# Performance work log

Measured on AMD Instinct MI355X. Metric: run time of the kernel, lower is better.

The kernel has to match this reference:

```python
import jax, jax.numpy as jnp
import numpy as np

D_MODEL = 1024
N_HEADS = 16
D_K = D_MODEL // N_HEADS


def setup_inputs() -> dict:
    key = jax.random.key(0)
    ks = jax.random.split(key, 12)
    B, S = 2, 2048
    scale = 1.0 / np.sqrt(D_MODEL)
    inp = {
        "query": jax.random.normal(ks[0], (B, S, D_MODEL), jnp.float32),
        "key": jax.random.normal(ks[1], (B, S, D_MODEL), jnp.float32),
        "value": jax.random.normal(ks[2], (B, S, D_MODEL), jnp.float32),
        "weights": jax.random.uniform(ks[3], (B, S), jnp.float32),
        "wq": jax.random.normal(ks[4], (D_MODEL, D_MODEL), jnp.float32) * scale,
        "bq": jnp.zeros((D_MODEL,), jnp.float32),
        "wk": jax.random.normal(ks[5], (D_MODEL, D_MODEL), jnp.float32) * scale,
        "bk": jnp.zeros((D_MODEL,), jnp.float32),
        "wv": jax.random.normal(ks[6], (D_MODEL, D_MODEL), jnp.float32) * scale,
        "bv": jnp.zeros((D_MODEL,), jnp.float32),
        "wo": jax.random.normal(ks[7], (D_MODEL, D_MODEL), jnp.float32) * scale,
        "bo": jnp.zeros((D_MODEL,), jnp.float32),
    }
    return inp


def _split_heads(x):
    # (B, S, d_model) -> (B, H, S, d_k)
    B, S, _ = x.shape
    return x.reshape(B, S, N_HEADS, D_K).transpose(0, 2, 1, 3)


def reference(query, key, value, weights, wq, bq, wk, bk, wv, bv, wo, bo):
    Q = _split_heads(query @ wq + bq)
    K = _split_heads(key @ wk + bk)
    V = _split_heads(value @ wv + bv)
    # scores: (B, H, n_q, n_kv)
    scores = jnp.einsum("bhqd,bhkd->bhqk", Q, K) / np.sqrt(D_K)
    log_w = jnp.log(weights + 1e-20)[:, None, None, :]  # (B,1,1,n_kv)
    attn = jax.nn.softmax(scores + log_w, axis=-1)
    out = jnp.einsum("bhqk,bhkd->bhqd", attn, V)
    B, H, S, Dk = out.shape
    out = out.transpose(0, 2, 1, 3).reshape(B, S, D_MODEL)
    return out @ wo + bo
```

## Files before the change

kernel.cpp:

```cpp
#include <hip/hip_runtime.h>

typedef unsigned short u16;
typedef __bf16 bf16x8 __attribute__((ext_vector_type(8)));
typedef float f32x4 __attribute__((ext_vector_type(4)));
typedef float f32x16 __attribute__((ext_vector_type(16)));

#define D_MODEL 1024
#define NH 16
#define DKD 64
#define BB 2
#define SS 2048
#define QSCL 0.18033688011112042f

#if __has_builtin(__builtin_amdgcn_exp2f)
#define EXP2(x) __builtin_amdgcn_exp2f(x)
#else
#define EXP2(x) exp2f(x)
#endif

__device__ __forceinline__ u16 f2bf(float f) {
  union { float f; unsigned u; } x; x.f = f;
  unsigned r = x.u + 0x7fffu + ((x.u >> 16) & 1u);
  return (u16)(r >> 16);
}

__device__ __forceinline__ void gld16(const u16* g, u16* l) {
  __builtin_amdgcn_global_load_lds((__attribute__((address_space(1))) void*)(g),
                                   (__attribute__((address_space(3))) void*)(l),
                                   16, 0, 0);
}

extern "C" __global__ void __launch_bounds__(256) kprep_conv(
    const float* __restrict__ q, const float* __restrict__ k, const float* __restrict__ v,
    u16* __restrict__ xq, u16* __restrict__ xk, u16* __restrict__ xv)
{
  int z = blockIdx.y;
  const float* s = z == 0 ? q : (z == 1 ? k : v);
  u16* d = z == 0 ? xq : (z == 1 ? xk : xv);
  int i = (blockIdx.x * 256 + threadIdx.x) * 4;
  float4 val = *(const float4*)(s + i);
  ushort4 o;
  o.x = f2bf(val.x); o.y = f2bf(val.y); o.z = f2bf(val.z); o.w = f2bf(val.w);
  *(ushort4*)(d + i) = o;
}

extern "C" __global__ void __launch_bounds__(256) kprep_wt(
    const float* __restrict__ w0, const float* __restrict__ w1,
    const float* __restrict__ w2, const float* __restrict__ w3,
    u16* __restrict__ o0, u16* __restrict__ o1, u16* __restrict__ o2, u16* __restrict__ o3)
{
  const float* src; u16* dst;
  switch (blockIdx.z) {
    case 0: src = w0; dst = o0; break;
    case 1: src = w1; dst = o1; break;
    case 2: src = w2; dst = o2; break;
    default: src = w3; dst = o3; break;
  }
  __shared__ float t[32][33];
  int n0 = blockIdx.x * 32, k0 = blockIdx.y * 32;
  int tx = threadIdx.x & 31, ty = threadIdx.x >> 5;
  #pragma unroll
  for (int i = 0; i < 32; i += 8)
    t[ty + i][tx] = src[(k0 + ty + i) * D_MODEL + n0 + tx];
  __syncthreads();
  #pragma unroll
  for (int i = 0; i < 32; i += 8)
    dst[(size_t)(n0 + ty + i) * D_MODEL + k0 + tx] = f2bf(t[tx][ty + i]);
}

extern "C" __global__ void __launch_bounds__(256) klw(
    const float* __restrict__ w, float* __restrict__ lw)
{
  int i = blockIdx.x * 256 + threadIdx.x;
  if (i < BB * SS) lw[i] = log2f(w[i] + 1e-20f) - 16.0f;
}

extern "C" __global__ void __launch_bounds__(256) ktrans_v(
    const u16* __restrict__ src, u16* __restrict__ dst)
{
  __shared__ u16 T[64][72];
  int bh = blockIdx.y; int s0 = blockIdx.x * 64;
  int tid = threadIdx.x;
  int r = tid >> 3, c = (tid & 7) * 8;
  #pragma unroll
  for (int i = 0; i < 2; ++i)
    *(bf16x8*)&T[r + i * 32][c] = *(const bf16x8*)&src[((size_t)bh * SS + s0 + r + i * 32) * DKD + c];
  __syncthreads();
  #pragma unroll
  for (int i = 0; i < 2; ++i) {
    int dk = r + i * 32;
    ushort4 o0, o1;
    o0.x = T[c + 0][dk]; o0.y = T[c + 1][dk]; o0.z = T[c + 2][dk]; o0.w = T[c + 3][dk];
    o1.x = T[c + 4][dk]; o1.y = T[c + 5][dk]; o1.z = T[c + 6][dk]; o1.w = T[c + 7][dk];
    *(ushort4*)&dst[((size_t)bh * DKD + dk) * SS + s0 + c] = o0;
    *(ushort4*)&dst[((size_t)bh * DKD + dk) * SS + s0 + c + 4] = o1;
  }
}

__device__ __forceinline__ void gemm_tile(const u16* __restrict__ Ag, const u16* __restrict__ Bg,
                                          u16* As, u16* Bs, f32x4 acc[4][4], int tid)
{
  int lane = tid & 63;
  int lr = lane & 15, lg = lane >> 4;
  int w = tid >> 6, wr = w >> 1, wc = w & 1;
  for (int k0 = 0; k0 < D_MODEL; k0 += 32) {
    #pragma unroll
    for (int c = 0; c < 2; ++c) {
      int idx = tid + c * 256;
      int row = idx >> 2, col = (idx & 3) * 8;
      gld16(Ag + row * D_MODEL + k0 + col, As + idx * 8);
      gld16(Bg + row * D_MODEL + k0 + col, Bs + idx * 8);
    }
    __syncthreads();
    bf16x8 af[4], bfr[4];
    #pragma unroll
    for (int mi = 0; mi < 4; ++mi)
      af[mi] = *(const bf16x8*)(As + (wr * 64 + mi * 16 + lr) * 32 + lg * 8);
    #pragma unroll
    for (int nj = 0; nj < 4; ++nj)
      bfr[nj] = *(const bf16x8*)(Bs + (wc * 64 + nj * 16 + lr) * 32 + lg * 8);
    #pragma unroll
    for (int mi = 0; mi < 4; ++mi)
      #pragma unroll
      for (int nj = 0; nj < 4; ++nj)
        acc[mi][nj] = __builtin_amdgcn_mfma_f32_16x16x32_bf16(af[mi], bfr[nj], acc[mi][nj], 0, 0, 0);
    __syncthreads();
  }
}

extern "C" __global__ void __launch_bounds__(256) kgemm_qkv(
    const u16* __restrict__ xq, const u16* __restrict__ xk, const u16* __restrict__ xv,
    const u16* __restrict__ wqt, const u16* __restrict__ wkt, const u16* __restrict__ wvt,
    const float* __restrict__ bq, const float* __restrict__ bk, const float* __restrict__ bv,
    u16* __restrict__ Qb, u16* __restrict__ Kb, u16* __restrict__ Vb)
{
  __shared__ u16 As[128 * 32], Bs[128 * 32];
  int z = blockIdx.z;
  const u16* X  = z == 0 ? xq : (z == 1 ? xk : xv);
  const u16* Wt = z == 0 ? wqt : (z == 1 ? wkt : wvt);
  const float* bias = z == 0 ? bq : (z == 1 ? bk : bv);
  u16* dst = z == 0 ? Qb : (z == 1 ? Kb : Vb);
  int tid = threadIdx.x;
  f32x4 zero = {0.f, 0.f, 0.f, 0.f};
  f32x4 acc[4][4];
  #pragma unroll
  for (int i = 0; i < 4; ++i)
    #pragma unroll
    for (int j = 0; j < 4; ++j) acc[i][j] = zero;
  int m0 = blockIdx.y * 128, n0 = blockIdx.x * 128;
  gemm_tile(X + (size_t)m0 * D_MODEL, Wt + (size_t)n0 * D_MODEL, As, Bs, acc, tid);
  int lane = tid & 63, lr = lane & 15, lg = lane >> 4;
  int w = tid >> 6, wr = w >> 1, wc = w & 1;
  float scl = (z == 0) ? QSCL : 1.0f;
  #pragma unroll
  for (int mi = 0; mi < 4; ++mi)
    #pragma unroll
    for (int nj = 0; nj < 4; ++nj) {
      int n = n0 + wc * 64 + nj * 16 + lr;
      float bs = bias[n];
      int h = n >> 6, dk = n & 63;
      #pragma unroll
      for (int j = 0; j < 4; ++j) {
        int m = m0 + wr * 64 + mi * 16 + lg * 4 + j;
        int b = m >> 11, s = m & 2047;
        dst[(((size_t)(b * NH + h)) * SS + s) * DKD + dk] = f2bf((acc[mi][nj][j] + bs) * scl);
      }
    }
}

extern "C" __global__ void __launch_bounds__(256) kgemm_o(
    const u16* __restrict__ AO, const u16* __restrict__ wot,
    const float* __restrict__ bo, float* __restrict__ out)
{
  __shared__ u16 As[128 * 32], Bs[128 * 32];
  int tid = threadIdx.x;
  f32x4 zero = {0.f, 0.f, 0.f, 0.f};
  f32x4 acc[4][4];
  #pragma unroll
  for (int i = 0; i < 4; ++i)
    #pragma unroll
    for (int j = 0; j < 4; ++j) acc[i][j] = zero;
  int m0 = blockIdx.y * 128, n0 = blockIdx.x * 128;
  gemm_tile(AO + (size_t)m0 * D_MODEL, wot + (size_t)n0 * D_MODEL, As, Bs, acc, tid);
  int lane = tid & 63, lr = lane & 15, lg = lane >> 4;
  int w = tid >> 6, wr = w >> 1, wc = w & 1;
  #pragma unroll
  for (int mi = 0; mi < 4; ++mi)
    #pragma unroll
    for (int nj = 0; nj < 4; ++nj) {
      int n = n0 + wc * 64 + nj * 16 + lr;
      float bs = bo[n];
      #pragma unroll
      for (int j = 0; j < 4; ++j) {
        int m = m0 + wr * 64 + mi * 16 + lg * 4 + j;
        out[(size_t)m * D_MODEL + n] = acc[mi][nj][j] + bs;
      }
    }
}

extern "C" __global__ void __launch_bounds__(256, 4) kattn(
    const u16* __restrict__ Qb, const u16* __restrict__ Kb, const u16* __restrict__ Vt,
    const float* __restrict__ lw2, u16* __restrict__ AO)
{
  __shared__ __align__(16) u16 Ks[2][64 * 64];
  __shared__ __align__(16) u16 Vs[2][64 * 64];
  __shared__ __align__(16) float lwf[SS];

  int tid = threadIdx.x, lane = tid & 63, w = tid >> 6;
  int lq = lane & 31, hi = lane >> 5;

  int n = blockIdx.x;
  int xcd = n & 7, slot = n >> 3;
  int bh = xcd + 8 * (slot >> 4);
  int q0 = (slot & 15) * 128;
  int b = bh >> 4, h = bh & 15;

  const u16* Qg = Qb + ((size_t)bh * SS + q0 + w * 32) * DKD;
  const u16* Kg = Kb + (size_t)bh * SS * DKD;
  const u16* Vg = Vt + (size_t)bh * DKD * SS;
  const float* lwb = lw2 + b * SS;

  #pragma unroll
  for (int i = 0; i < 2; ++i) {
    int idx = tid + i * 256;
    *(float4*)&lwf[idx * 4] = *(const float4*)(lwb + idx * 4);
  }

  bf16x8 qf[4];
  #pragma unroll
  for (int kc = 0; kc < 4; ++kc)
    qf[kc] = *(const bf16x8*)(Qg + lq * DKD + kc * 16 + hi * 8);

  f32x16 acco[2] = {};
  float lsp[4] = {0.f, 0.f, 0.f, 0.f};

  int srow0 = tid >> 3, sc0 = ((tid & 7) ^ (srow0 & 7)) * 8;
  int srow1 = srow0 + 32, sc1 = ((tid & 7) ^ (srow1 & 7)) * 8;

#define STAGE(t, bi) do { \
    gld16(Kg + (size_t)((t) * 64 + srow0) * DKD + sc0, &Ks[bi][tid * 8]); \
    gld16(Kg + (size_t)((t) * 64 + srow1) * DKD + sc1, &Ks[bi][(tid + 256) * 8]); \
    gld16(Vg + (size_t)srow0 * SS + (t) * 64 + sc0, &Vs[bi][tid * 8]); \
    gld16(Vg + (size_t)srow1 * SS + (t) * 64 + sc1, &Vs[bi][(tid + 256) * 8]); \
  } while (0)

  const int NT = SS / 64;
  STAGE(0, 0);
  for (int t = 0; t < NT; ++t) {
    asm volatile("s_waitcnt vmcnt(0) lgkmcnt(0)" ::: "memory");
    __builtin_amdgcn_s_barrier();
    __builtin_amdgcn_sched_barrier(0);
    if (t + 1 < NT) STAGE(t + 1, (t + 1) & 1);
    int bi = t & 1;
    int kv0 = t * 64;

    f32x16 st[2];
    #pragma unroll
    for (int nh = 0; nh < 2; ++nh)
      #pragma unroll
      for (int g = 0; g < 4; ++g) {
        f32x4 lv = *(const f32x4*)&lwf[kv0 + nh * 32 + 4 * hi + 8 * g];
        st[nh][4 * g + 0] = lv[0]; st[nh][4 * g + 1] = lv[1];
        st[nh][4 * g + 2] = lv[2]; st[nh][4 * g + 3] = lv[3];
      }

    __builtin_amdgcn_s_setprio(1);
    #pragma unroll
    for (int kc = 0; kc < 4; ++kc) {
      bf16x8 kf0 = *(const bf16x8*)&Ks[bi][(lq) * 64      + (((kc * 2 + hi) ^ (lq & 7)) * 8)];
      bf16x8 kf1 = *(const bf16x8*)&Ks[bi][(32 + lq) * 64 + (((kc * 2 + hi) ^ (lq & 7)) * 8)];
      st[0] = __builtin_amdgcn_mfma_f32_32x32x16_bf16(kf0, qf[kc], st[0], 0, 0, 0);
      st[1] = __builtin_amdgcn_mfma_f32_32x32x16_bf16(kf1, qf[kc], st[1], 0, 0, 0);
    }
    __builtin_amdgcn_s_setprio(0);

    unsigned wd[2][8];
    #pragma unroll
    for (int nh = 0; nh < 2; ++nh)
      #pragma unroll
      for (int r2 = 0; r2 < 8; ++r2) {
        float plo = EXP2(st[nh][2 * r2]);
        float phi = EXP2(st[nh][2 * r2 + 1]);
        lsp[r2 & 3] += plo + phi;
        union { unsigned u; __bf16 b2[2]; } cv;
        cv.b2[0] = (__bf16)plo; cv.b2[1] = (__bf16)phi;
        wd[nh][r2] = cv.u;
      }

    bf16x8 Pb[4];
    #pragma unroll
    for (int c = 0; c < 4; ++c) {
      int nh = c >> 1, j0 = 4 * (c & 1);
      auto s1 = __builtin_amdgcn_permlane32_swap(wd[nh][j0 + 0], wd[nh][j0 + 2], false, false);
      auto s2 = __builtin_amdgcn_permlane32_swap(wd[nh][j0 + 1], wd[nh][j0 + 3], false, false);
      union { unsigned u[4]; bf16x8 v; } pb;
      pb.u[0] = s1[0]; pb.u[1] = s2[0]; pb.u[2] = s1[1]; pb.u[3] = s2[1];
      Pb[c] = pb.v;
    }

    __builtin_amdgcn_s_setprio(1);
    #pragma unroll
    for (int c = 0; c < 4; ++c) {
      bf16x8 vf0 = *(const bf16x8*)&Vs[bi][(lq) * 64      + (((c * 2 + hi) ^ (lq & 7)) * 8)];
      bf16x8 vf1 = *(const bf16x8*)&Vs[bi][(32 + lq) * 64 + (((c * 2 + hi) ^ (lq & 7)) * 8)];
      acco[0] = __builtin_amdgcn_mfma_f32_32x32x16_bf16(vf0, Pb[c], acco[0], 0, 0, 0);
      acco[1] = __builtin_amdgcn_mfma_f32_32x32x16_bf16(vf1, Pb[c], acco[1], 0, 0, 0);
    }
    __builtin_amdgcn_s_setprio(0);
  }
#undef STAGE

  float lsum = (lsp[0] + lsp[1]) + (lsp[2] + lsp[3]);
  lsum += __shfl_xor(lsum, 32);
  float inv = 1.0f / lsum;
  int s = q0 + w * 32 + lq;
  size_t base = ((size_t)b * SS + s) * D_MODEL + h * DKD;
  #pragma unroll
  for (int dh = 0; dh < 2; ++dh)
    #pragma unroll
    for (int g = 0; g < 4; ++g) {
      ushort4 o;
      o.x = f2bf(acco[dh][4 * g + 0] * inv);
      o.y = f2bf(acco[dh][4 * g + 1] * inv);
      o.z = f2bf(acco[dh][4 * g + 2] * inv);
      o.w = f2bf(acco[dh][4 * g + 3] * inv);
      *(ushort4*)(AO + base + dh * 32 + 4 * hi + 8 * g) = o;
    }
}

extern "C" void kernel_launch(void* const* d_in, const int* in_sizes, int n_in,
                              void* d_out, int out_size, void* d_ws, size_t ws_size,
                              hipStream_t stream) {
  const float* query = (const float*)d_in[0];
  const float* key_  = (const float*)d_in[1];
  const float* value = (const float*)d_in[2];
  const float* wts   = (const float*)d_in[3];
  const float* wq = (const float*)d_in[4];
  const float* bq = (const float*)d_in[5];
  const float* wk = (const float*)d_in[6];
  const float* bk = (const float*)d_in[7];
  const float* wv = (const float*)d_in[8];
  const float* bv = (const float*)d_in[9];
  const float* wo = (const float*)d_in[10];
  const float* bo = (const float*)d_in[11];
  float* out = (float*)d_out;

  char* ws = (char*)d_ws;
  const size_t MB = 1024 * 1024;
  u16* Xq  = (u16*)(ws + 0 * MB);
  u16* Xk  = (u16*)(ws + 8 * MB);
  u16* Xv  = (u16*)(ws + 16 * MB);
  u16* WqT = (u16*)(ws + 24 * MB);
  u16* WkT = (u16*)(ws + 26 * MB);
  u16* WvT = (u16*)(ws + 28 * MB);
  u16* WoT = (u16*)(ws + 30 * MB);
  u16* Qb  = (u16*)(ws + 32 * MB);
  u16* Kb  = (u16*)(ws + 40 * MB);
  u16* Vb  = (u16*)(ws + 48 * MB);
  u16* AO  = (u16*)(ws + 56 * MB);
  float* lwbuf = (float*)(ws + 64 * MB);
  u16* VtT = (u16*)(ws + 16 * MB);

  kprep_conv<<<dim3(4096, 3), 256, 0, stream>>>(query, key_, value, Xq, Xk, Xv);
  kprep_wt<<<dim3(32, 32, 4), 256, 0, stream>>>(wq, wk, wv, wo, WqT, WkT, WvT, WoT);
  klw<<<16, 256, 0, stream>>>(wts, lwbuf);
  kgemm_qkv<<<dim3(8, 32, 3), 256, 0, stream>>>(Xq, Xk, Xv, WqT, WkT, WvT, bq, bk, bv, Qb, Kb, Vb);
  ktrans_v<<<dim3(32, 32), 256, 0, stream>>>(Vb, VtT);
  kattn<<<512, 256, 0, stream>>>(Qb, Kb, VtT, lwbuf, AO);
  kgemm_o<<<dim3(8, 32), 256, 0, stream>>>(AO, WoT, bo, out);
}
```

Before: 139.9 us.

## Split KV loop across two wave groups in attention and fuse log-weight prep

The attention kernel now runs 512 threads per block, with two groups of four waves each processing alternate KV tiles for the same queries. Partial accumulators and row sums are combined through shared memory at the end. K/V staging moves to a four-slot ring with a deeper prefetch. The separate log-weight kernel is folded into an extra block of the conversion kernel to save a launch. This should raise latency hiding and in-flight memory traffic, at the cost of more shared memory, an extra barrier per iteration and a final reduction.

```diff
diff --git a/kernel.cpp b/kernel.cpp
--- a/kernel.cpp
+++ b/kernel.cpp
@@ -32,9 +32,25 @@
 
 extern "C" __global__ void __launch_bounds__(256) kprep_conv(
     const float* __restrict__ q, const float* __restrict__ k, const float* __restrict__ v,
-    u16* __restrict__ xq, u16* __restrict__ xk, u16* __restrict__ xv)
+    const float* __restrict__ wts,
+    u16* __restrict__ xq, u16* __restrict__ xk, u16* __restrict__ xv,
+    float* __restrict__ lw)
 {
   int z = blockIdx.y;
+  if (blockIdx.x == 4096) {
+    if (z == 0) {
+      int i = threadIdx.x * 16;
+      #pragma unroll
+      for (int j = 0; j < 16; j += 4) {
+        float4 val = *(const float4*)(wts + i + j);
+        lw[i + j + 0] = log2f(val.x + 1e-20f) - 16.0f;
+        lw[i + j + 1] = log2f(val.y + 1e-20f) - 16.0f;
+        lw[i + j + 2] = log2f(val.z + 1e-20f) - 16.0f;
+        lw[i + j + 3] = log2f(val.w + 1e-20f) - 16.0f;
+      }
+    }
+    return;
+  }
   const float* s = z == 0 ? q : (z == 1 ? k : v);
   u16* d = z == 0 ? xq : (z == 1 ? xk : xv);
   int i = (blockIdx.x * 256 + threadIdx.x) * 4;
@@ -66,13 +82,6 @@
   #pragma unroll
   for (int i = 0; i < 32; i += 8)
     dst[(size_t)(n0 + ty + i) * D_MODEL + k0 + tx] = f2bf(t[tx][ty + i]);
-}
-
-extern "C" __global__ void __launch_bounds__(256) klw(
-    const float* __restrict__ w, float* __restrict__ lw)
-{
-  int i = blockIdx.x * 256 + threadIdx.x;
-  if (i < BB * SS) lw[i] = log2f(w[i] + 1e-20f) - 16.0f;
 }
 
 extern "C" __global__ void __launch_bounds__(256) ktrans_v(
@@ -198,16 +207,16 @@
     }
 }
 
-extern "C" __global__ void __launch_bounds__(256, 4) kattn(
+extern "C" __global__ void __launch_bounds__(512, 4) kattn(
     const u16* __restrict__ Qb, const u16* __restrict__ Kb, const u16* __restrict__ Vt,
     const float* __restrict__ lw2, u16* __restrict__ AO)
 {
-  __shared__ __align__(16) u16 Ks[2][64 * 64];
-  __shared__ __align__(16) u16 Vs[2][64 * 64];
-  __shared__ __align__(16) float lwf[SS];
+  __shared__ __align__(16) char smem[4 * 16384 + 8192];
+  float* lwf = (float*)(smem + 65536);
 
   int tid = threadIdx.x, lane = tid & 63, w = tid >> 6;
   int lq = lane & 31, hi = lane >> 5;
+  int qw = w & 3, par = w >> 2;
 
   int n = blockIdx.x;
   int xcd = n & 7, slot = n >> 3;
@@ -215,16 +224,12 @@
   int q0 = (slot & 15) * 128;
   int b = bh >> 4, h = bh & 15;
 
-  const u16* Qg = Qb + ((size_t)bh * SS + q0 + w * 32) * DKD;
+  const u16* Qg = Qb + ((size_t)bh * SS + q0 + qw * 32) * DKD;
   const u16* Kg = Kb + (size_t)bh * SS * DKD;
   const u16* Vg = Vt + (size_t)bh * DKD * SS;
   const float* lwb = lw2 + b * SS;
 
-  #pragma unroll
-  for (int i = 0; i < 2; ++i) {
-    int idx = tid + i * 256;
-    *(float4*)&lwf[idx * 4] = *(const float4*)(lwb + idx * 4);
-  }
+  *(float4*)&lwf[tid * 4] = *(const float4*)(lwb + tid * 4);
 
   bf16x8 qf[4];
   #pragma unroll
@@ -234,25 +239,27 @@
   f32x16 acco[2] = {};
   float lsp[4] = {0.f, 0.f, 0.f, 0.f};
 
-  int srow0 = tid >> 3, sc0 = ((tid & 7) ^ (srow0 & 7)) * 8;
-  int srow1 = srow0 + 32, sc1 = ((tid & 7) ^ (srow1 & 7)) * 8;
-
-#define STAGE(t, bi) do { \
-    gld16(Kg + (size_t)((t) * 64 + srow0) * DKD + sc0, &Ks[bi][tid * 8]); \
-    gld16(Kg + (size_t)((t) * 64 + srow1) * DKD + sc1, &Ks[bi][(tid + 256) * 8]); \
-    gld16(Vg + (size_t)srow0 * SS + (t) * 64 + sc0, &Vs[bi][tid * 8]); \
-    gld16(Vg + (size_t)srow1 * SS + (t) * 64 + sc1, &Vs[bi][(tid + 256) * 8]); \
+  int srow = tid >> 3, sc = ((tid & 7) ^ (srow & 7)) * 8;
+
+#define KSLOT(sl) ((u16*)(smem + (sl) * 16384))
+#define VSLOT(sl) ((u16*)(smem + (sl) * 16384 + 8192))
+#define STAGE(t, sl) do { \
+    gld16(Kg + (size_t)((t) * 64 + srow) * DKD + sc, KSLOT(sl) + tid * 8); \
+    gld16(Vg + (size_t)srow * SS + (t) * 64 + sc, VSLOT(sl) + tid * 8); \
   } while (0)
 
-  const int NT = SS / 64;
-  STAGE(0, 0);
-  for (int t = 0; t < NT; ++t) {
-    asm volatile("s_waitcnt vmcnt(0) lgkmcnt(0)" ::: "memory");
+  STAGE(0, 0); STAGE(1, 1); STAGE(2, 2); STAGE(3, 3);
+  for (int i = 0; i < 16; ++i) {
+    if (i < 15) asm volatile("s_waitcnt vmcnt(4) lgkmcnt(0)" ::: "memory");
+    else        asm volatile("s_waitcnt vmcnt(0) lgkmcnt(0)" ::: "memory");
     __builtin_amdgcn_s_barrier();
     __builtin_amdgcn_sched_barrier(0);
-    if (t + 1 < NT) STAGE(t + 1, (t + 1) & 1);
-    int bi = t & 1;
+
+    int t = 2 * i + par;
+    int bi = t & 3;
     int kv0 = t * 64;
+    const u16* Kp = KSLOT(bi);
+    const u16* Vp = VSLOT(bi);
 
     f32x16 st[2];
     #pragma unroll
@@ -267,8 +274,8 @@
     __builtin_amdgcn_s_setprio(1);
     #pragma unroll
     for (int kc = 0; kc < 4; ++kc) {
-      bf16x8 kf0 = *(const bf16x8*)&Ks[bi][(lq) * 64      + (((kc * 2 + hi) ^ (lq & 7)) * 8)];
-      bf16x8 kf1 = *(const bf16x8*)&Ks[bi][(32 + lq) * 64 + (((kc * 2 + hi) ^ (lq & 7)) * 8)];
+      bf16x8 kf0 = *(const bf16x8*)&Kp[(lq) * 64      + (((kc * 2 + hi) ^ (lq & 7)) * 8)];
+      bf16x8 kf1 = *(const bf16x8*)&Kp[(32 + lq) * 64 + (((kc * 2 + hi) ^ (lq & 7)) * 8)];
       st[0] = __builtin_amdgcn_mfma_f32_32x32x16_bf16(kf0, qf[kc], st[0], 0, 0, 0);
       st[1] = __builtin_amdgcn_mfma_f32_32x32x16_bf16(kf1, qf[kc], st[1], 0, 0, 0);
     }
@@ -301,31 +308,59 @@
     __builtin_amdgcn_s_setprio(1);
     #pragma unroll
     for (int c = 0; c < 4; ++c) {
-      bf16x8 vf0 = *(const bf16x8*)&Vs[bi][(lq) * 64      + (((c * 2 + hi) ^ (lq & 7)) * 8)];
-      bf16x8 vf1 = *(const bf16x8*)&Vs[bi][(32 + lq) * 64 + (((c * 2 + hi) ^ (lq & 7)) * 8)];
+      bf16x8 vf0 = *(const bf16x8*)&Vp[(lq) * 64      + (((c * 2 + hi) ^ (lq & 7)) * 8)];
+      bf16x8 vf1 = *(const bf16x8*)&Vp[(32 + lq) * 64 + (((c * 2 + hi) ^ (lq & 7)) * 8)];
       acco[0] = __builtin_amdgcn_mfma_f32_32x32x16_bf16(vf0, Pb[c], acco[0], 0, 0, 0);
       acco[1] = __builtin_amdgcn_mfma_f32_32x32x16_bf16(vf1, Pb[c], acco[1], 0, 0, 0);
     }
     __builtin_amdgcn_s_setprio(0);
+
+    __builtin_amdgcn_sched_barrier(0);
+    __builtin_amdgcn_s_barrier();
+    int tn = 2 * i + 4;
+    if (tn < 32) { STAGE(tn, tn & 3); STAGE(tn + 1, (tn + 1) & 3); }
   }
 #undef STAGE
 
-  float lsum = (lsp[0] + lsp[1]) + (lsp[2] + lsp[3]);
-  lsum += __shfl_xor(lsum, 32);
-  float inv = 1.0f / lsum;
-  int s = q0 + w * 32 + lq;
-  size_t base = ((size_t)b * SS + s) * D_MODEL + h * DKD;
-  #pragma unroll
-  for (int dh = 0; dh < 2; ++dh)
-    #pragma unroll
-    for (int g = 0; g < 4; ++g) {
-      ushort4 o;
-      o.x = f2bf(acco[dh][4 * g + 0] * inv);
-      o.y = f2bf(acco[dh][4 * g + 1] * inv);
-      o.z = f2bf(acco[dh][4 * g + 2] * inv);
-      o.w = f2bf(acco[dh][4 * g + 3] * inv);
-      *(ushort4*)(AO + base + dh * 32 + 4 * hi + 8 * g) = o;
-    }
+  float lsum_part = (lsp[0] + lsp[1]) + (lsp[2] + lsp[3]);
+  float* comb = (float*)smem;
+  int coff = (qw * 64 + lane) * 34;
+  if (par == 1) {
+    #pragma unroll
+    for (int d = 0; d < 2; ++d)
+      #pragma unroll
+      for (int g = 0; g < 8; ++g)
+        *(float2*)&comb[coff + (d * 8 + g) * 2] = make_float2(acco[d][2 * g], acco[d][2 * g + 1]);
+    comb[coff + 32] = lsum_part;
+  }
+  __syncthreads();
+  if (par == 0) {
+    #pragma unroll
+    for (int d = 0; d < 2; ++d)
+      #pragma unroll
+      for (int g = 0; g < 8; ++g) {
+        float2 v = *(const float2*)&comb[coff + (d * 8 + g) * 2];
+        acco[d][2 * g] += v.x; acco[d][2 * g + 1] += v.y;
+      }
+    lsum_part += comb[coff + 32];
+    float lsum = lsum_part + __shfl_xor(lsum_part, 32);
+    float inv = 1.0f / lsum;
+    int s = q0 + qw * 32 + lq;
+    size_t base = ((size_t)b * SS + s) * D_MODEL + h * DKD;
+    #pragma unroll
+    for (int dh = 0; dh < 2; ++dh)
+      #pragma unroll
+      for (int g = 0; g < 4; ++g) {
+        ushort4 o;
+        o.x = f2bf(acco[dh][4 * g + 0] * inv);
+        o.y = f2bf(acco[dh][4 * g + 1] * inv);
+        o.z = f2bf(acco[dh][4 * g + 2] * inv);
+        o.w = f2bf(acco[dh][4 * g + 3] * inv);
+        *(ushort4*)(AO + base + dh * 32 + 4 * hi + 8 * g) = o;
+      }
+  }
+#undef KSLOT
+#undef VSLOT
 }
 
 extern "C" void kernel_launch(void* const* d_in, const int* in_sizes, int n_in,
@@ -361,11 +396,10 @@
   float* lwbuf = (float*)(ws + 64 * MB);
   u16* VtT = (u16*)(ws + 16 * MB);
 
-  kprep_conv<<<dim3(4096, 3), 256, 0, stream>>>(query, key_, value, Xq, Xk, Xv);
+  kprep_conv<<<dim3(4097, 3), 256, 0, stream>>>(query, key_, value, wts, Xq, Xk, Xv, lwbuf);
   kprep_wt<<<dim3(32, 32, 4), 256, 0, stream>>>(wq, wk, wv, wo, WqT, WkT, WvT, WoT);
-  klw<<<16, 256, 0, stream>>>(wts, lwbuf);
   kgemm_qkv<<<dim3(8, 32, 3), 256, 0, stream>>>(Xq, Xk, Xv, WqT, WkT, WvT, bq, bk, bv, Qb, Kb, Vb);
   ktrans_v<<<dim3(32, 32), 256, 0, stream>>>(Vb, VtT);
-  kattn<<<512, 256, 0, stream>>>(Qb, Kb, VtT, lwbuf, AO);
+  kattn<<<512, 512, 0, stream>>>(Qb, Kb, VtT, lwbuf, AO);
   kgemm_o<<<dim3(8, 32), 256, 0, stream>>>(AO, WoT, bo, out);
 }
```

Result: faster. 134.9 us (-3.6%).
